# Kernel optimization log

Measured on AMD Instinct MI355X. Metric: run time of the kernel, lower is better.

## Reference

```python
import jax, jax.numpy as jnp
import numpy as np

L = 512       # sequence length
N_AA = 21     # amino-acid alphabet size
D = 128       # per-residue substitution embedding dim
N1 = 256
N2 = 256


def setup_inputs() -> dict:
    key = jax.random.key(0)
    k1, k2, k3 = jax.random.split(key, 3)
    X1 = jax.random.randint(k1, (N1, L), 0, N_AA)
    X2 = jax.random.randint(k2, (N2, L), 0, N_AA)
    W = jax.random.normal(k3, (L * N_AA, N_AA * D), dtype=jnp.float32) * 0.02
    b = jnp.zeros((N_AA * D,), jnp.float32)
    w_param = jnp.zeros((L * (L - 1) // 2,), jnp.float32)
    a = jnp.ones((1,), jnp.float32)
    return {"X1": X1, "X2": X2, "W": W, "b": b, "w_param": w_param, "a": a}


def _network(X, W, b):
    # one-hot + linear stand-in for self.network; outputs (n, n_aa, d)
    n = X.shape[0]
    oh = jax.nn.one_hot(X, N_AA, dtype=W.dtype).reshape(n, -1)  # (n, L*n_aa)
    return (oh @ W + b).reshape(n, N_AA, -1)


def _wdk(subs, w):
    # torch: (subs[:, graph] * w).sum(2) * subs, summed over dim 1
    # graph[i] = arange(L), so this equals subs @ w^T contracted with subs:
    # out[..] = sum_i sum_j subs[.., i] * w[i, j] * subs[.., j]
    return jnp.einsum('...i,ij,...j->...', subs, w, subs)


def reference(X1, X2, W, b, w_param, a):
    n1, Lx = X1.shape
    n2 = X2.shape[0]

    # symmetric pairwise weight matrix; diagonal stays 0 -> sigmoid(0)=0.5
    i_x, i_y = np.tril_indices(Lx, k=-1)
    wm = jnp.zeros((Lx, Lx), W.dtype).at[i_x, i_y].set(w_param).at[i_y, i_x].set(w_param)
    w = jax.nn.sigmoid(wm)

    # per-sequence substitution matrices S = E E^T, (n, n_aa, n_aa)
    E1 = _network(X1, W, b)
    S1 = jnp.einsum('nad,nbd->nab', E1, E1)
    E2 = _network(X2, W, b)
    S2 = jnp.einsum('nad,nbd->nab', E2, E2)

    r1 = jnp.arange(n1)
    r2 = jnp.arange(n2)

    # self terms: subs[n, l] = S[n, X[n,l], X[n,l]]
    d1 = S1[r1[:, None], X1, X1]                  # (n1, L)
    k1 = _wdk(d1, w)[:, None]                     # (n1, 1)
    d2 = S2[r2[:, None], X2, X2]                  # (n2, L)
    k2 = _wdk(d2, w)[None, :]                     # (1, n2)

    # cross terms: average of the two sequences' S, gathered directly
    # (avoids materializing the (n1*n2, n_aa, n_aa) averaged S tensor)
    g1 = S1[r1[:, None, None], X1[:, None, :], X2[None, :, :]]  # (n1, n2, L)
    g2 = S2[r2[None, :, None], X1[:, None, :], X2[None, :, :]]  # (n1, n2, L)
    subs = 0.5 * (g1 + g2)

    K = _wdk(subs, w)                             # (n1, n2)
    K = K / jnp.sqrt(k1) / jnp.sqrt(k2)
    return (a ** 2) * K
```

## Files before the change

kernel.cpp:

```cpp
#include <hip/hip_runtime.h>
#include <cstdint>
#include <cstddef>

typedef __attribute__((ext_vector_type(8))) __bf16 bf16x8;
typedef __attribute__((ext_vector_type(4))) float f32x4;
typedef __attribute__((ext_vector_type(16))) float f32x16;

__device__ __forceinline__ unsigned short f2b(float x) {
    uint32_t u = __float_as_uint(x);
    u += 0x7FFFu + ((u >> 16) & 1u);
    return (unsigned short)(u >> 16);
}
__device__ __forceinline__ float b2f(unsigned short h) {
    return __uint_as_float(((uint32_t)h) << 16);
}

#define L_SEQ 512
#define N_AA 21
#define DDIM 128
#define NCOL 2688
#define NSEQ 512
#define TBSTRIDE 448
#define KTOT 10752
#define KWORDS_TOT 336
#define ZCH 12
#define KCHUNK 896
#define KWORDS 28
#define KBTOT 672
#define NFRAG 56448

#define PB_WBZ   14112
#define PB_EINIT 5376
#define PB_REPACK 1024
#define PB_WBUILD 1024
#define PB_ABITS 672
#define PB_TOTAL (PB_WBZ + PB_EINIT + PB_REPACK + PB_WBUILD + PB_ABITS)

__global__ __launch_bounds__(256) void prep_kernel(const int* X1, const int* X2,
                                                   const float* W, const float* bvec, const float* wp,
                                                   uint8_t* X8, uint32_t* Abits,
                                                   float* w32, unsigned short* wswz,
                                                   float* E, unsigned short* Wbz) {
    int bid = blockIdx.x;
    int t = threadIdx.x;
    if (bid < PB_WBZ) {
        int f = bid * 4 + (t >> 6);
        int lane = t & 63, lr = lane & 31, hf = lane >> 5;
        int cb = f / KBTOT, kb = f - cb * KBTOT;
        const float* src = W + (size_t)(kb * 16 + hf * 8) * NCOL + cb * 32 + lr;
        union { uint4 q; unsigned short s[8]; } o;
#pragma unroll
        for (int j = 0; j < 8; ++j) o.s[j] = f2b(src[(size_t)j * NCOL]);
        *(uint4*)&Wbz[(size_t)f * 512 + lane * 8] = o.q;
        return;
    }
    bid -= PB_WBZ;
    if (bid < PB_EINIT) {
        int e = bid * 256 + t;
        E[e] = bvec[e % NCOL];
        return;
    }
    bid -= PB_EINIT;
    if (bid < PB_REPACK) {
        int e = bid * 256 + t;
        if (e < 131072) X8[e] = (uint8_t)X1[e];
        else            X8[e] = (uint8_t)X2[e - 131072];
        return;
    }
    bid -= PB_REPACK;
    if (bid < PB_WBUILD) {
        int e = bid * 256 + t;
        int p = e >> 9, q = e & 511;
        float x = 0.0f;
        if (p > q)      x = wp[p * (p - 1) / 2 + q];
        else if (p < q) x = wp[q * (q - 1) / 2 + p];
        float s = 1.0f / (1.0f + expf(-x));
        w32[e] = s;
        int nb = p >> 5, lr = p & 31;
        int kb = q >> 4, hf = (q >> 3) & 1, j = q & 7;
        wswz[(size_t)((nb * 32 + kb) * 512) + (hf * 32 + lr) * 8 + j] = f2b(s);
        return;
    }
    bid -= PB_WBUILD;
    {
        int e = bid * 256 + t;
        if (e >= NSEQ * KWORDS_TOT) return;
        int seq = e / KWORDS_TOT, w = e - seq * KWORDS_TOT;
        int k0 = w * 32;
        int l_lo = k0 / N_AA;
        int l_hi = (k0 + 31) / N_AA;
        if (l_hi > L_SEQ - 1) l_hi = L_SEQ - 1;
        uint32_t bits = 0;
        for (int l = l_lo; l <= l_hi; ++l) {
            int aa = (seq < 256) ? X1[(size_t)seq * L_SEQ + l]
                                 : X2[(size_t)(seq - 256) * L_SEQ + l];
            int pos = l * N_AA + aa - k0;
            if (pos >= 0 && pos < 32) bits |= (1u << pos);
        }
        Abits[e] = bits;
    }
}

__global__ __launch_bounds__(256) void e_mfma_bz_kernel(const uint32_t* Abits, const unsigned short* Wbz, float* E) {
    __shared__ uint32_t Ab[256 * 29];
    int t = threadIdx.x;
    int c0 = blockIdx.x * 128;
    int m0 = blockIdx.y * 256;
    int w0 = blockIdx.z * KWORDS;

    for (int idx = t; idx < 256 * KWORDS; idx += 256) {
        int r = idx / KWORDS, w = idx - r * KWORDS;
        Ab[r * 29 + w] = Abits[(size_t)(m0 + r) * KWORDS_TOT + w0 + w];
    }
    __syncthreads();

    int wid = t >> 6, lane = t & 63;
    int lr = lane & 31, hf = lane >> 5;
    int mbase = (wid & 1) * 128;

    f32x16 acc[4][2];
#pragma unroll
    for (int s = 0; s < 4; ++s)
#pragma unroll
        for (int o = 0; o < 2; ++o)
#pragma unroll
            for (int r = 0; r < 16; ++r) acc[s][o][r] = 0.f;

    int kb0 = blockIdx.z * (KCHUNK / 16);
    const unsigned short* Bz0 = Wbz + (size_t)(((c0 >> 5) + (wid >> 1) * 2 + 0) * KBTOT + kb0) * 512 + lane * 8;
    const unsigned short* Bz1 = Wbz + (size_t)(((c0 >> 5) + (wid >> 1) * 2 + 1) * KBTOT + kb0) * 512 + lane * 8;

#pragma unroll 2
    for (int ks = 0; ks < KCHUNK / 16; ++ks) {
        int word = ks >> 1;
        int b0 = (ks & 1) * 16 + hf * 8;
        bf16x8 afrag[4];
#pragma unroll
        for (int s = 0; s < 4; ++s) {
            uint32_t bits = Ab[(mbase + s * 32 + lr) * 29 + word];
            uint32_t bb = (bits >> b0) & 0xFFu;
            union { bf16x8 v; uint32_t u[4]; } af;
#pragma unroll
            for (int p = 0; p < 4; ++p) {
                uint32_t u = 0;
                if ((bb >> (2 * p)) & 1u)     u |= 0x3F80u;
                if ((bb >> (2 * p + 1)) & 1u) u |= 0x3F800000u;
                af.u[p] = u;
            }
            afrag[s] = af.v;
        }
        bf16x8 bv0 = *(const bf16x8*)(Bz0 + ks * 512);
        bf16x8 bv1 = *(const bf16x8*)(Bz1 + ks * 512);
#pragma unroll
        for (int s = 0; s < 4; ++s) {
            acc[s][0] = __builtin_amdgcn_mfma_f32_32x32x16_bf16(afrag[s], bv0, acc[s][0], 0, 0, 0);
            acc[s][1] = __builtin_amdgcn_mfma_f32_32x32x16_bf16(afrag[s], bv1, acc[s][1], 0, 0, 0);
        }
    }

#pragma unroll
    for (int s = 0; s < 4; ++s)
#pragma unroll
        for (int o = 0; o < 2; ++o)
#pragma unroll
            for (int r = 0; r < 16; ++r) {
                int row = (r & 3) + 8 * (r >> 2) + 4 * hf;
                float* dst = E + (size_t)(m0 + mbase + s * 32 + row) * NCOL + c0 + ((wid >> 1) * 2) * 32 + (((r >> 4) == 0) ? 0 : 0);
                (void)dst;
                float* dst2 = E + (size_t)(m0 + mbase + s * 32 + row) * NCOL + c0 + ((wid >> 1) * 2 + o) * 32 + lr;
                atomicAdd(dst2, acc[s][o][r]);
            }
}

__global__ __launch_bounds__(256) void t_kernel(const float* E, unsigned short* Tb, float* Tdiag) {
    __shared__ float4 Es4[21 * 33];
    int t = threadIdx.x, n = blockIdx.x;
    for (int e = t; e < 21 * 32; e += 256) {
        int r = e >> 5, d = e & 31;
        Es4[r * 33 + d] = *(const float4*)(E + (size_t)n * NCOL + r * 128 + d * 4);
    }
    __syncthreads();
    for (int e = t; e < 441; e += 256) {
        int r = e / 21, c = e - r * 21;
        const float4* ar = &Es4[r * 33];
        const float4* br = &Es4[c * 33];
        float s = 0.f;
#pragma unroll 8
        for (int d = 0; d < 32; ++d) {
            float4 a = ar[d], b = br[d];
            s += a.x * b.x + a.y * b.y + a.z * b.z + a.w * b.w;
        }
        Tb[(size_t)n * TBSTRIDE + e] = f2b(0.5f * s);
        if (r == c) Tdiag[n * 24 + r] = s;
    }
}

__global__ __launch_bounds__(256) void k_kernel(const uint8_t* X8, const float* Tdiag, const float* w32, float* kinv) {
    __shared__ __align__(16) float dvec[4][512];
    __shared__ float Td[4][21];
    __shared__ float red[4][256];
    int t = threadIdx.x, n0 = blockIdx.x * 4;
    if (t < 84) Td[t / 21][t % 21] = Tdiag[(size_t)(n0 + t / 21) * 24 + (t % 21)];
    __syncthreads();
    for (int e = t; e < 2048; e += 256) {
        int nn = e >> 9, l = e & 511;
        dvec[nn][l] = Td[nn][X8[(size_t)(n0 + nn) * 512 + l]];
    }
    __syncthreads();
    float p0 = 0.f, p1 = 0.f, p2 = 0.f, p3 = 0.f;
    for (int p = t; p < 512; p += 256) {
        const float4* wr4 = (const float4*)(w32 + (size_t)p * 512);
        float d0 = 0.f, d1 = 0.f, d2 = 0.f, d3 = 0.f;
        for (int q = 0; q < 128; ++q) {
            float4 wv = wr4[q];
            float4 a = ((const float4*)dvec[0])[q];
            float4 b = ((const float4*)dvec[1])[q];
            float4 c = ((const float4*)dvec[2])[q];
            float4 d = ((const float4*)dvec[3])[q];
            d0 += wv.x * a.x + wv.y * a.y + wv.z * a.z + wv.w * a.w;
            d1 += wv.x * b.x + wv.y * b.y + wv.z * b.z + wv.w * b.w;
            d2 += wv.x * c.x + wv.y * c.y + wv.z * c.z + wv.w * c.w;
            d3 += wv.x * d.x + wv.y * d.y + wv.z * d.z + wv.w * d.w;
        }
        p0 += dvec[0][p] * d0;
        p1 += dvec[1][p] * d1;
        p2 += dvec[2][p] * d2;
        p3 += dvec[3][p] * d3;
    }
    red[0][t] = p0; red[1][t] = p1; red[2][t] = p2; red[3][t] = p3;
    __syncthreads();
    for (int s = 128; s > 0; s >>= 1) {
        if (t < s) {
            red[0][t] += red[0][t + s];
            red[1][t] += red[1][t + s];
            red[2][t] += red[2][t + s];
            red[3][t] += red[3][t + s];
        }
        __syncthreads();
    }
    if (t < 4) kinv[n0 + t] = 1.0f / sqrtf(red[t][0]);
}

__global__ __launch_bounds__(512, 6) void k4_kernel(const uint8_t* X8, const unsigned short* Tb,
                                                    const unsigned short* wswz, const float* kinv,
                                                    const float* Ainp, float* out) {
    __shared__ unsigned short Sh[32 * 520];
    __shared__ unsigned short Ts1h[4 * TBSTRIDE];
    __shared__ unsigned short Ts2h[8 * TBSTRIDE];
    __shared__ unsigned short A21[4 * 512];
    __shared__ uint8_t Xs2[8 * 512];
    __shared__ float Kacc[8][32];

    int t = threadIdx.x;
    int i0 = blockIdx.x * 4;
    int j0 = blockIdx.y * 8;

    for (int e = t; e < 4 * 512; e += 512)
        A21[e] = (unsigned short)(21 * X8[(size_t)(i0 + (e >> 9)) * 512 + (e & 511)]);
    {
        const uint32_t* s2 = (const uint32_t*)(X8 + (size_t)(256 + j0) * 512);
        uint32_t* d2 = (uint32_t*)Xs2;
        for (int e = t; e < 1024; e += 512) d2[e] = s2[e];
    }
    {
        uint32_t* d1 = (uint32_t*)Ts1h;
        for (int e = t; e < 4 * 224; e += 512) {
            int r = e / 224, w = e - r * 224;
            d1[e] = ((const uint32_t*)(Tb + (size_t)(i0 + r) * TBSTRIDE))[w];
        }
        uint32_t* d2 = (uint32_t*)Ts2h;
        for (int e = t; e < 8 * 224; e += 512) {
            int r = e / 224, w = e - r * 224;
            d2[e] = ((const uint32_t*)(Tb + (size_t)(256 + j0 + r) * TBSTRIDE))[w];
        }
    }
    __syncthreads();

    for (int e4 = t; e4 < 32 * 128; e4 += 512) {
        int pr = e4 >> 7, p = (e4 & 127) * 4;
        int ti = pr >> 3, tj = pr & 7;
        uint64_t a4 = *(const uint64_t*)&A21[ti * 512 + p];
        uint32_t b4 = *(const uint32_t*)&Xs2[tj * 512 + p];
        const unsigned short* T1 = &Ts1h[ti * TBSTRIDE];
        const unsigned short* T2 = &Ts2h[tj * TBSTRIDE];
        uint64_t outw = 0;
#pragma unroll
        for (int u = 0; u < 4; ++u) {
            int idx = (int)((a4 >> (16 * u)) & 0xFFFFu) + (int)((b4 >> (8 * u)) & 0xFFu);
            float v = b2f(T1[idx]) + b2f(T2[idx]);
            outw |= (uint64_t)f2b(v) << (16 * u);
        }
        *(uint64_t*)&Sh[pr * 520 + p] = outw;
    }
    __syncthreads();

    int wid = t >> 6, lane = t & 63;
    int lr = lane & 31, hf = lane >> 5;
    int n_base = wid * 64;

    const unsigned short* Sa = &Sh[lr * 520 + hf * 8];
    const unsigned short* Bz0 = wswz + (size_t)((wid * 2 + 0) * 32) * 512 + lane * 8;
    const unsigned short* Bz1 = wswz + (size_t)((wid * 2 + 1) * 32) * 512 + lane * 8;

    f32x16 acc0, acc1;
#pragma unroll
    for (int j = 0; j < 16; ++j) { acc0[j] = 0.f; acc1[j] = 0.f; }

#pragma unroll 2
    for (int kt = 0; kt < 32; ++kt) {
        bf16x8 av = *(const bf16x8*)(Sa + kt * 16);
        bf16x8 bv0 = *(const bf16x8*)(Bz0 + kt * 512);
        bf16x8 bv1 = *(const bf16x8*)(Bz1 + kt * 512);
        acc0 = __builtin_amdgcn_mfma_f32_32x32x16_bf16(av, bv0, acc0, 0, 0, 0);
        acc1 = __builtin_amdgcn_mfma_f32_32x32x16_bf16(av, bv1, acc1, 0, 0, 0);
    }

    float prow[16];
#pragma unroll
    for (int r = 0; r < 16; ++r) {
        int row = (r & 3) + 8 * (r >> 2) + 4 * hf;
        float v = acc0[r] * b2f(Sh[row * 520 + (n_base + lr)]);
        v      += acc1[r] * b2f(Sh[row * 520 + (n_base + 32 + lr)]);
        prow[r] = v;
    }
#pragma unroll
    for (int r = 0; r < 16; ++r) {
        float v = prow[r];
        v += __shfl_xor(v, 1);
        v += __shfl_xor(v, 2);
        v += __shfl_xor(v, 4);
        v += __shfl_xor(v, 8);
        v += __shfl_xor(v, 16);
        if (lr == 0) {
            int row = (r & 3) + 8 * (r >> 2) + 4 * hf;
            Kacc[wid][row] = v;
        }
    }
    __syncthreads();

    if (t < 32) {
        float K = Kacc[0][t] + Kacc[1][t] + Kacc[2][t] + Kacc[3][t]
                + Kacc[4][t] + Kacc[5][t] + Kacc[6][t] + Kacc[7][t];
        int ti = t >> 3, tj = t & 7;
        int i = i0 + ti, j = j0 + tj;
        float a0 = Ainp[0];
        out[i * 256 + j] = a0 * a0 * K * kinv[i] * kinv[256 + j];
    }
}

extern "C" void kernel_launch(void* const* d_in, const int* in_sizes, int n_in,
                              void* d_out, int out_size, void* d_ws, size_t ws_size,
                              hipStream_t stream) {
    const int*   X1 = (const int*)d_in[0];
    const int*   X2 = (const int*)d_in[1];
    const float* W  = (const float*)d_in[2];
    const float* b  = (const float*)d_in[3];
    const float* wp = (const float*)d_in[4];
    const float* a  = (const float*)d_in[5];
    float* out = (float*)d_out;

    char* ws = (char*)d_ws;
    float*          E     = (float*)(ws + 0);
    unsigned short* Tb    = (unsigned short*)(ws + 5505024);
    float*          Tdiag = (float*)(ws + 5963776);
    float*          w32   = (float*)(ws + 6012928);
    unsigned short* wswz  = (unsigned short*)(ws + 7061504);
    float*          kinv  = (float*)(ws + 7585792);
    uint8_t*        X8    = (uint8_t*)(ws + 7587840);
    uint32_t*       Abits = (uint32_t*)(ws + 7849984);
    unsigned short* Wbz   = (unsigned short*)(ws + 8538112);

    prep_kernel<<<PB_TOTAL, 256, 0, stream>>>(X1, X2, W, b, wp, X8, Abits, w32, wswz, E, Wbz);
    e_mfma_bz_kernel<<<dim3(21, 2, ZCH), 256, 0, stream>>>(Abits, Wbz, E);
    t_kernel<<<512, 256, 0, stream>>>(E, Tb, Tdiag);
    k_kernel<<<128, 256, 0, stream>>>(X8, Tdiag, w32, kinv);
    k4_kernel<<<dim3(64, 32), 512, 0, stream>>>(X8, Tb, wswz, kinv, a, out);
}
```

Measured before the change: 370.2 us.

## Materialize one-hot A as pre-swizzled bf16 fragments and retile the embedding GMM

The embedding GEMM kernel no longer expands a packed bitmask into bf16 A fragments inside the MFMA loop. The prep kernel now writes the one-hot matrix directly in MFMA fragment order as bf16, about 11 MB. The new GEMM launches 1008 blocks over 64x64 warp tiles with 56 k-steps each, reads A and B fragments straight from global memory, uses an XCD-aware block remap, and sets a higher occupancy bound. This removes the per-step ALU and LDS decode work, but adds extra global traffic for A and more atomic adds because the K split is finer.

```diff
diff --git a/kernel.cpp b/kernel.cpp
--- a/kernel.cpp
+++ b/kernel.cpp
@@ -22,25 +22,22 @@
 #define NSEQ 512
 #define TBSTRIDE 448
 #define KTOT 10752
-#define KWORDS_TOT 336
 #define ZCH 12
-#define KCHUNK 896
-#define KWORDS 28
 #define KBTOT 672
-#define NFRAG 56448
+#define KBCH 56
 
 #define PB_WBZ   14112
 #define PB_EINIT 5376
 #define PB_REPACK 1024
 #define PB_WBUILD 1024
-#define PB_ABITS 672
-#define PB_TOTAL (PB_WBZ + PB_EINIT + PB_REPACK + PB_WBUILD + PB_ABITS)
+#define PB_ABZ   2688
+#define PB_TOTAL (PB_WBZ + PB_EINIT + PB_REPACK + PB_WBUILD + PB_ABZ)
 
 __global__ __launch_bounds__(256) void prep_kernel(const int* X1, const int* X2,
                                                    const float* W, const float* bvec, const float* wp,
-                                                   uint8_t* X8, uint32_t* Abits,
+                                                   uint8_t* X8,
                                                    float* w32, unsigned short* wswz,
-                                                   float* E, unsigned short* Wbz) {
+                                                   float* E, unsigned short* Wbz, unsigned short* Abz) {
     int bid = blockIdx.x;
     int t = threadIdx.x;
     if (bid < PB_WBZ) {
@@ -83,93 +80,69 @@
     }
     bid -= PB_WBUILD;
     {
-        int e = bid * 256 + t;
-        if (e >= NSEQ * KWORDS_TOT) return;
-        int seq = e / KWORDS_TOT, w = e - seq * KWORDS_TOT;
-        int k0 = w * 32;
-        int l_lo = k0 / N_AA;
-        int l_hi = (k0 + 31) / N_AA;
-        if (l_hi > L_SEQ - 1) l_hi = L_SEQ - 1;
-        uint32_t bits = 0;
-        for (int l = l_lo; l <= l_hi; ++l) {
-            int aa = (seq < 256) ? X1[(size_t)seq * L_SEQ + l]
-                                 : X2[(size_t)(seq - 256) * L_SEQ + l];
-            int pos = l * N_AA + aa - k0;
-            if (pos >= 0 && pos < 32) bits |= (1u << pos);
-        }
-        Abits[e] = bits;
-    }
-}
-
-__global__ __launch_bounds__(256) void e_mfma_bz_kernel(const uint32_t* Abits, const unsigned short* Wbz, float* E) {
-    __shared__ uint32_t Ab[256 * 29];
-    int t = threadIdx.x;
-    int c0 = blockIdx.x * 128;
-    int m0 = blockIdx.y * 256;
-    int w0 = blockIdx.z * KWORDS;
-
-    for (int idx = t; idx < 256 * KWORDS; idx += 256) {
-        int r = idx / KWORDS, w = idx - r * KWORDS;
-        Ab[r * 29 + w] = Abits[(size_t)(m0 + r) * KWORDS_TOT + w0 + w];
-    }
-    __syncthreads();
-
-    int wid = t >> 6, lane = t & 63;
+        int f = bid * 4 + (t >> 6);
+        int lane = t & 63, lr = lane & 31, hf = lane >> 5;
+        int mb = f / KBTOT, kb = f - mb * KBTOT;
+        int m = mb * 32 + lr;
+        const int* Xrow = (m < 256) ? (X1 + (size_t)m * L_SEQ) : (X2 + (size_t)(m - 256) * L_SEQ);
+        int k0 = kb * 16 + hf * 8;
+        union { uint4 q; unsigned short s[8]; } o;
+#pragma unroll
+        for (int j = 0; j < 8; ++j) {
+            int k = k0 + j;
+            int l = k / N_AA;
+            int aa = k - l * N_AA;
+            o.s[j] = (Xrow[l] == aa) ? (unsigned short)0x3F80u : (unsigned short)0u;
+        }
+        *(uint4*)&Abz[(size_t)f * 512 + lane * 8] = o.q;
+    }
+}
+
+__global__ __launch_bounds__(256, 4) void e_mfma_v2(const unsigned short* Abz, const unsigned short* Wbz, float* E) {
+    int lin = blockIdx.x;
+    int s = ((lin & 7) * 126) + (lin >> 3);
+    int cx = s % 21;
+    int rem = s / 21;
+    int my = rem & 3;
+    int kz = rem >> 2;
+
+    int t = threadIdx.x, wid = t >> 6, lane = t & 63;
     int lr = lane & 31, hf = lane >> 5;
-    int mbase = (wid & 1) * 128;
-
-    f32x16 acc[4][2];
-#pragma unroll
-    for (int s = 0; s < 4; ++s)
-#pragma unroll
-        for (int o = 0; o < 2; ++o)
-#pragma unroll
-            for (int r = 0; r < 16; ++r) acc[s][o][r] = 0.f;
-
-    int kb0 = blockIdx.z * (KCHUNK / 16);
-    const unsigned short* Bz0 = Wbz + (size_t)(((c0 >> 5) + (wid >> 1) * 2 + 0) * KBTOT + kb0) * 512 + lane * 8;
-    const unsigned short* Bz1 = Wbz + (size_t)(((c0 >> 5) + (wid >> 1) * 2 + 1) * KBTOT + kb0) * 512 + lane * 8;
+
+    int kb0 = kz * KBCH;
+    int mb0 = my * 4 + (wid & 1) * 2;
+    int cb0 = cx * 4 + (wid >> 1) * 2;
+
+    const unsigned short* Ap0 = Abz + ((size_t)(mb0 * KBTOT + kb0)) * 512 + lane * 8;
+    const unsigned short* Ap1 = Ap0 + (size_t)KBTOT * 512;
+    const unsigned short* Bp0 = Wbz + ((size_t)(cb0 * KBTOT + kb0)) * 512 + lane * 8;
+    const unsigned short* Bp1 = Bp0 + (size_t)KBTOT * 512;
+
+    f32x16 acc00, acc01, acc10, acc11;
+#pragma unroll
+    for (int r = 0; r < 16; ++r) { acc00[r] = 0.f; acc01[r] = 0.f; acc10[r] = 0.f; acc11[r] = 0.f; }
 
 #pragma unroll 2
-    for (int ks = 0; ks < KCHUNK / 16; ++ks) {
-        int word = ks >> 1;
-        int b0 = (ks & 1) * 16 + hf * 8;
-        bf16x8 afrag[4];
-#pragma unroll
-        for (int s = 0; s < 4; ++s) {
-            uint32_t bits = Ab[(mbase + s * 32 + lr) * 29 + word];
-            uint32_t bb = (bits >> b0) & 0xFFu;
-            union { bf16x8 v; uint32_t u[4]; } af;
-#pragma unroll
-            for (int p = 0; p < 4; ++p) {
-                uint32_t u = 0;
-                if ((bb >> (2 * p)) & 1u)     u |= 0x3F80u;
-                if ((bb >> (2 * p + 1)) & 1u) u |= 0x3F800000u;
-                af.u[p] = u;
-            }
-            afrag[s] = af.v;
-        }
-        bf16x8 bv0 = *(const bf16x8*)(Bz0 + ks * 512);
-        bf16x8 bv1 = *(const bf16x8*)(Bz1 + ks * 512);
-#pragma unroll
-        for (int s = 0; s < 4; ++s) {
-            acc[s][0] = __builtin_amdgcn_mfma_f32_32x32x16_bf16(afrag[s], bv0, acc[s][0], 0, 0, 0);
-            acc[s][1] = __builtin_amdgcn_mfma_f32_32x32x16_bf16(afrag[s], bv1, acc[s][1], 0, 0, 0);
-        }
-    }
-
-#pragma unroll
-    for (int s = 0; s < 4; ++s)
-#pragma unroll
-        for (int o = 0; o < 2; ++o)
-#pragma unroll
-            for (int r = 0; r < 16; ++r) {
-                int row = (r & 3) + 8 * (r >> 2) + 4 * hf;
-                float* dst = E + (size_t)(m0 + mbase + s * 32 + row) * NCOL + c0 + ((wid >> 1) * 2) * 32 + (((r >> 4) == 0) ? 0 : 0);
-                (void)dst;
-                float* dst2 = E + (size_t)(m0 + mbase + s * 32 + row) * NCOL + c0 + ((wid >> 1) * 2 + o) * 32 + lr;
-                atomicAdd(dst2, acc[s][o][r]);
-            }
+    for (int kb = 0; kb < KBCH; ++kb) {
+        bf16x8 a0 = *(const bf16x8*)(Ap0 + kb * 512);
+        bf16x8 a1 = *(const bf16x8*)(Ap1 + kb * 512);
+        bf16x8 b0 = *(const bf16x8*)(Bp0 + kb * 512);
+        bf16x8 b1 = *(const bf16x8*)(Bp1 + kb * 512);
+        acc00 = __builtin_amdgcn_mfma_f32_32x32x16_bf16(a0, b0, acc00, 0, 0, 0);
+        acc01 = __builtin_amdgcn_mfma_f32_32x32x16_bf16(a0, b1, acc01, 0, 0, 0);
+        acc10 = __builtin_amdgcn_mfma_f32_32x32x16_bf16(a1, b0, acc10, 0, 0, 0);
+        acc11 = __builtin_amdgcn_mfma_f32_32x32x16_bf16(a1, b1, acc11, 0, 0, 0);
+    }
+
+#pragma unroll
+    for (int r = 0; r < 16; ++r) {
+        int row = (r & 3) + 8 * (r >> 2) + 4 * hf;
+        float* base = E + (size_t)(mb0 * 32 + row) * NCOL + cb0 * 32 + lr;
+        atomicAdd(base, acc00[r]);
+        atomicAdd(base + 32, acc01[r]);
+        atomicAdd(base + (size_t)32 * NCOL, acc10[r]);
+        atomicAdd(base + (size_t)32 * NCOL + 32, acc11[r]);
+    }
 }
 
 __global__ __launch_bounds__(256) void t_kernel(const float* E, unsigned short* Tb, float* Tdiag) {
@@ -367,11 +340,11 @@
     unsigned short* wswz  = (unsigned short*)(ws + 7061504);
     float*          kinv  = (float*)(ws + 7585792);
     uint8_t*        X8    = (uint8_t*)(ws + 7587840);
-    uint32_t*       Abits = (uint32_t*)(ws + 7849984);
-    unsigned short* Wbz   = (unsigned short*)(ws + 8538112);
-
-    prep_kernel<<<PB_TOTAL, 256, 0, stream>>>(X1, X2, W, b, wp, X8, Abits, w32, wswz, E, Wbz);
-    e_mfma_bz_kernel<<<dim3(21, 2, ZCH), 256, 0, stream>>>(Abits, Wbz, E);
+    unsigned short* Abz   = (unsigned short*)(ws + 7849984);
+    unsigned short* Wbz   = (unsigned short*)(ws + 18860032);
+
+    prep_kernel<<<PB_TOTAL, 256, 0, stream>>>(X1, X2, W, b, wp, X8, w32, wswz, E, Wbz, Abz);
+    e_mfma_v2<<<1008, 256, 0, stream>>>(Abz, Wbz, E);
     t_kernel<<<512, 256, 0, stream>>>(E, Tb, Tdiag);
     k_kernel<<<128, 256, 0, stream>>>(X8, Tdiag, w32, kinv);
     k4_kernel<<<dim3(64, 32), 512, 0, stream>>>(X8, Tb, wswz, kinv, a, out);
```

Measured after the change: 382.7 us. 3.4% more time.

## Retile E matmul with prefetched B and XCD-aware grid; coalesce k_kernel

Applied to the files above, without the earlier changes.

The one-hot embedding GEMM kernel switches from 252 blocks of 256x128 tiles to 1008 blocks of 128x128 tiles. Block indices are remapped so neighbouring blocks are spread across XCDs, and B fragments are software-prefetched four k-steps ahead to hide load latency. Separately, the self-term kernel now has 512 threads, each handling 8 contiguous columns, so w rows are read coalesced and reduced with wave shuffles. This adds more atomicAdd traffic from the smaller tiles in exchange for more parallelism and latency hiding.

```diff
diff --git a/kernel.cpp b/kernel.cpp
--- a/kernel.cpp
+++ b/kernel.cpp
@@ -23,11 +23,10 @@
 #define TBSTRIDE 448
 #define KTOT 10752
 #define KWORDS_TOT 336
+#define KWORDS 28
 #define ZCH 12
-#define KCHUNK 896
-#define KWORDS 28
 #define KBTOT 672
-#define NFRAG 56448
+#define KBCH 56
 
 #define PB_WBZ   14112
 #define PB_EINIT 5376
@@ -101,75 +100,84 @@
     }
 }
 
-__global__ __launch_bounds__(256) void e_mfma_bz_kernel(const uint32_t* Abits, const unsigned short* Wbz, float* E) {
-    __shared__ uint32_t Ab[256 * 29];
-    int t = threadIdx.x;
-    int c0 = blockIdx.x * 128;
-    int m0 = blockIdx.y * 256;
-    int w0 = blockIdx.z * KWORDS;
-
-    for (int idx = t; idx < 256 * KWORDS; idx += 256) {
+__global__ __launch_bounds__(256, 4) void e_mfma_v4(const uint32_t* Abits, const unsigned short* Wbz, float* E) {
+    __shared__ uint32_t Ab[128 * 29];
+
+    int lin = blockIdx.x;
+    int s_ = ((lin & 7) * 126) + (lin >> 3);
+    int cx = s_ % 21;
+    int rem = s_ / 21;
+    int my = rem & 3;
+    int kz = rem >> 2;
+
+    int t = threadIdx.x, wid = t >> 6, lane = t & 63;
+    int lr = lane & 31, hf = lane >> 5, hf8 = hf * 8;
+    int m0 = my * 128;
+    int w0 = kz * KWORDS;
+    int kb0 = kz * KBCH;
+
+    for (int idx = t; idx < 128 * KWORDS; idx += 256) {
         int r = idx / KWORDS, w = idx - r * KWORDS;
         Ab[r * 29 + w] = Abits[(size_t)(m0 + r) * KWORDS_TOT + w0 + w];
     }
     __syncthreads();
 
-    int wid = t >> 6, lane = t & 63;
-    int lr = lane & 31, hf = lane >> 5;
-    int mbase = (wid & 1) * 128;
-
-    f32x16 acc[4][2];
-#pragma unroll
-    for (int s = 0; s < 4; ++s)
-#pragma unroll
-        for (int o = 0; o < 2; ++o)
-#pragma unroll
-            for (int r = 0; r < 16; ++r) acc[s][o][r] = 0.f;
-
-    int kb0 = blockIdx.z * (KCHUNK / 16);
-    const unsigned short* Bz0 = Wbz + (size_t)(((c0 >> 5) + (wid >> 1) * 2 + 0) * KBTOT + kb0) * 512 + lane * 8;
-    const unsigned short* Bz1 = Wbz + (size_t)(((c0 >> 5) + (wid >> 1) * 2 + 1) * KBTOT + kb0) * 512 + lane * 8;
-
-#pragma unroll 2
-    for (int ks = 0; ks < KCHUNK / 16; ++ks) {
-        int word = ks >> 1;
-        int b0 = (ks & 1) * 16 + hf * 8;
-        bf16x8 afrag[4];
-#pragma unroll
-        for (int s = 0; s < 4; ++s) {
-            uint32_t bits = Ab[(mbase + s * 32 + lr) * 29 + word];
-            uint32_t bb = (bits >> b0) & 0xFFu;
-            union { bf16x8 v; uint32_t u[4]; } af;
-#pragma unroll
-            for (int p = 0; p < 4; ++p) {
-                uint32_t u = 0;
-                if ((bb >> (2 * p)) & 1u)     u |= 0x3F80u;
-                if ((bb >> (2 * p + 1)) & 1u) u |= 0x3F800000u;
-                af.u[p] = u;
-            }
-            afrag[s] = af.v;
-        }
-        bf16x8 bv0 = *(const bf16x8*)(Bz0 + ks * 512);
-        bf16x8 bv1 = *(const bf16x8*)(Bz1 + ks * 512);
-#pragma unroll
-        for (int s = 0; s < 4; ++s) {
-            acc[s][0] = __builtin_amdgcn_mfma_f32_32x32x16_bf16(afrag[s], bv0, acc[s][0], 0, 0, 0);
-            acc[s][1] = __builtin_amdgcn_mfma_f32_32x32x16_bf16(afrag[s], bv1, acc[s][1], 0, 0, 0);
-        }
-    }
-
-#pragma unroll
-    for (int s = 0; s < 4; ++s)
-#pragma unroll
-        for (int o = 0; o < 2; ++o)
-#pragma unroll
-            for (int r = 0; r < 16; ++r) {
-                int row = (r & 3) + 8 * (r >> 2) + 4 * hf;
-                float* dst = E + (size_t)(m0 + mbase + s * 32 + row) * NCOL + c0 + ((wid >> 1) * 2) * 32 + (((r >> 4) == 0) ? 0 : 0);
-                (void)dst;
-                float* dst2 = E + (size_t)(m0 + mbase + s * 32 + row) * NCOL + c0 + ((wid >> 1) * 2 + o) * 32 + lr;
-                atomicAdd(dst2, acc[s][o][r]);
-            }
+    int cb = cx * 4 + wid;
+    const unsigned short* Bp = Wbz + ((size_t)(cb * KBTOT + kb0)) * 512 + lane * 8;
+
+    f32x16 acc0, acc1, acc2, acc3;
+#pragma unroll
+    for (int r = 0; r < 16; ++r) { acc0[r] = 0.f; acc1[r] = 0.f; acc2[r] = 0.f; acc3[r] = 0.f; }
+
+    bf16x8 br0 = *(const bf16x8*)(Bp + 0 * 512);
+    bf16x8 br1 = *(const bf16x8*)(Bp + 1 * 512);
+    bf16x8 br2 = *(const bf16x8*)(Bp + 2 * 512);
+    bf16x8 br3 = *(const bf16x8*)(Bp + 3 * 512);
+
+#define AFRAG(S, WORD, SH) ({ \
+        uint32_t bits_ = Ab[((S) * 32 + lr) * 29 + (WORD)]; \
+        uint32_t bb_ = (bits_ >> (SH)) & 0xFFu; \
+        union { bf16x8 v; uint32_t u[4]; } af_; \
+        af_.u[0] = ((bb_ & 1u)   ? 0x3F80u : 0u) | ((bb_ & 2u)   ? 0x3F800000u : 0u); \
+        af_.u[1] = ((bb_ & 4u)   ? 0x3F80u : 0u) | ((bb_ & 8u)   ? 0x3F800000u : 0u); \
+        af_.u[2] = ((bb_ & 16u)  ? 0x3F80u : 0u) | ((bb_ & 32u)  ? 0x3F800000u : 0u); \
+        af_.u[3] = ((bb_ & 64u)  ? 0x3F80u : 0u) | ((bb_ & 128u) ? 0x3F800000u : 0u); \
+        af_.v; })
+
+#define STEP(BV, KB) do { \
+        int word_ = (KB) >> 1; \
+        int sh_ = ((KB) & 1) * 16 + hf8; \
+        acc0 = __builtin_amdgcn_mfma_f32_32x32x16_bf16(AFRAG(0, word_, sh_), BV, acc0, 0, 0, 0); \
+        acc1 = __builtin_amdgcn_mfma_f32_32x32x16_bf16(AFRAG(1, word_, sh_), BV, acc1, 0, 0, 0); \
+        acc2 = __builtin_amdgcn_mfma_f32_32x32x16_bf16(AFRAG(2, word_, sh_), BV, acc2, 0, 0, 0); \
+        acc3 = __builtin_amdgcn_mfma_f32_32x32x16_bf16(AFRAG(3, word_, sh_), BV, acc3, 0, 0, 0); \
+    } while (0)
+
+#pragma unroll 1
+    for (int kb = 0; kb < 48; kb += 4) {
+        STEP(br0, kb + 0); br0 = *(const bf16x8*)(Bp + (size_t)(kb + 4) * 512);
+        STEP(br1, kb + 1); br1 = *(const bf16x8*)(Bp + (size_t)(kb + 5) * 512);
+        STEP(br2, kb + 2); br2 = *(const bf16x8*)(Bp + (size_t)(kb + 6) * 512);
+        STEP(br3, kb + 3); br3 = *(const bf16x8*)(Bp + (size_t)(kb + 7) * 512);
+    }
+    STEP(br0, 48); br0 = *(const bf16x8*)(Bp + 52 * 512);
+    STEP(br1, 49); br1 = *(const bf16x8*)(Bp + 53 * 512);
+    STEP(br2, 50); br2 = *(const bf16x8*)(Bp + 54 * 512);
+    STEP(br3, 51); br3 = *(const bf16x8*)(Bp + 55 * 512);
+    STEP(br0, 52); STEP(br1, 53); STEP(br2, 54); STEP(br3, 55);
+
+#undef STEP
+#undef AFRAG
+
+#pragma unroll
+    for (int r = 0; r < 16; ++r) {
+        int row = (r & 3) + 8 * (r >> 2) + 4 * hf;
+        float* b0p = E + (size_t)(m0 + row) * NCOL + cb * 32 + lr;
+        atomicAdd(b0p, acc0[r]);
+        atomicAdd(b0p + 32 * NCOL, acc1[r]);
+        atomicAdd(b0p + 64 * NCOL, acc2[r]);
+        atomicAdd(b0p + 96 * NCOL, acc3[r]);
+    }
 }
 
 __global__ __launch_bounds__(256) void t_kernel(const float* E, unsigned short* Tb, float* Tdiag) {
@@ -195,50 +203,64 @@
     }
 }
 
-__global__ __launch_bounds__(256) void k_kernel(const uint8_t* X8, const float* Tdiag, const float* w32, float* kinv) {
+__global__ __launch_bounds__(512) void k_kernel(const uint8_t* X8, const float* Tdiag, const float* w32, float* kinv) {
     __shared__ __align__(16) float dvec[4][512];
     __shared__ float Td[4][21];
-    __shared__ float red[4][256];
+    __shared__ float wred[4][8];
     int t = threadIdx.x, n0 = blockIdx.x * 4;
     if (t < 84) Td[t / 21][t % 21] = Tdiag[(size_t)(n0 + t / 21) * 24 + (t % 21)];
     __syncthreads();
-    for (int e = t; e < 2048; e += 256) {
+    for (int e = t; e < 2048; e += 512) {
         int nn = e >> 9, l = e & 511;
         dvec[nn][l] = Td[nn][X8[(size_t)(n0 + nn) * 512 + l]];
     }
     __syncthreads();
-    float p0 = 0.f, p1 = 0.f, p2 = 0.f, p3 = 0.f;
-    for (int p = t; p < 512; p += 256) {
-        const float4* wr4 = (const float4*)(w32 + (size_t)p * 512);
-        float d0 = 0.f, d1 = 0.f, d2 = 0.f, d3 = 0.f;
-        for (int q = 0; q < 128; ++q) {
-            float4 wv = wr4[q];
-            float4 a = ((const float4*)dvec[0])[q];
-            float4 b = ((const float4*)dvec[1])[q];
-            float4 c = ((const float4*)dvec[2])[q];
-            float4 d = ((const float4*)dvec[3])[q];
-            d0 += wv.x * a.x + wv.y * a.y + wv.z * a.z + wv.w * a.w;
-            d1 += wv.x * b.x + wv.y * b.y + wv.z * b.z + wv.w * b.w;
-            d2 += wv.x * c.x + wv.y * c.y + wv.z * c.z + wv.w * c.w;
-            d3 += wv.x * d.x + wv.y * d.y + wv.z * d.z + wv.w * d.w;
-        }
-        p0 += dvec[0][p] * d0;
-        p1 += dvec[1][p] * d1;
-        p2 += dvec[2][p] * d2;
-        p3 += dvec[3][p] * d3;
-    }
-    red[0][t] = p0; red[1][t] = p1; red[2][t] = p2; red[3][t] = p3;
-    __syncthreads();
-    for (int s = 128; s > 0; s >>= 1) {
-        if (t < s) {
-            red[0][t] += red[0][t + s];
-            red[1][t] += red[1][t + s];
-            red[2][t] += red[2][t + s];
-            red[3][t] += red[3][t + s];
-        }
-        __syncthreads();
-    }
-    if (t < 4) kinv[n0 + t] = 1.0f / sqrtf(red[t][0]);
+    int wid = t >> 6, lane = t & 63;
+    int q0 = lane * 8;
+
+    float4 dA0 = *(const float4*)&dvec[0][q0], dA1 = *(const float4*)&dvec[0][q0 + 4];
+    float4 dB0 = *(const float4*)&dvec[1][q0], dB1 = *(const float4*)&dvec[1][q0 + 4];
+    float4 dC0 = *(const float4*)&dvec[2][q0], dC1 = *(const float4*)&dvec[2][q0 + 4];
+    float4 dD0 = *(const float4*)&dvec[3][q0], dD1 = *(const float4*)&dvec[3][q0 + 4];
+
+    float4 rA0 = {0,0,0,0}, rA1 = {0,0,0,0}, rB0 = {0,0,0,0}, rB1 = {0,0,0,0};
+    float4 rC0 = {0,0,0,0}, rC1 = {0,0,0,0}, rD0 = {0,0,0,0}, rD1 = {0,0,0,0};
+
+#define FMA4(R, W, S) do { (R).x += (W).x * (S); (R).y += (W).y * (S); (R).z += (W).z * (S); (R).w += (W).w * (S); } while (0)
+    for (int p = wid; p < 512; p += 8) {
+        const float4* wr = (const float4*)(w32 + (size_t)p * 512 + q0);
+        float4 w0v = wr[0], w1v = wr[1];
+        float a = dvec[0][p], b = dvec[1][p], c = dvec[2][p], d = dvec[3][p];
+        FMA4(rA0, w0v, a); FMA4(rA1, w1v, a);
+        FMA4(rB0, w0v, b); FMA4(rB1, w1v, b);
+        FMA4(rC0, w0v, c); FMA4(rC1, w1v, c);
+        FMA4(rD0, w0v, d); FMA4(rD1, w1v, d);
+    }
+#undef FMA4
+
+#define DOT8(R0, R1, D0, D1) ((R0).x*(D0).x + (R0).y*(D0).y + (R0).z*(D0).z + (R0).w*(D0).w + \
+                              (R1).x*(D1).x + (R1).y*(D1).y + (R1).z*(D1).z + (R1).w*(D1).w)
+    float s0 = DOT8(rA0, rA1, dA0, dA1);
+    float s1 = DOT8(rB0, rB1, dB0, dB1);
+    float s2 = DOT8(rC0, rC1, dC0, dC1);
+    float s3 = DOT8(rD0, rD1, dD0, dD1);
+#undef DOT8
+
+#pragma unroll
+    for (int off = 1; off < 64; off <<= 1) {
+        s0 += __shfl_xor(s0, off);
+        s1 += __shfl_xor(s1, off);
+        s2 += __shfl_xor(s2, off);
+        s3 += __shfl_xor(s3, off);
+    }
+    if (lane == 0) { wred[0][wid] = s0; wred[1][wid] = s1; wred[2][wid] = s2; wred[3][wid] = s3; }
+    __syncthreads();
+    if (t < 4) {
+        float kk = 0.f;
+#pragma unroll
+        for (int w = 0; w < 8; ++w) kk += wred[t][w];
+        kinv[n0 + t] = 1.0f / sqrtf(kk);
+    }
 }
 
 __global__ __launch_bounds__(512, 6) void k4_kernel(const uint8_t* X8, const unsigned short* Tb,
@@ -371,8 +393,8 @@
     unsigned short* Wbz   = (unsigned short*)(ws + 8538112);
 
     prep_kernel<<<PB_TOTAL, 256, 0, stream>>>(X1, X2, W, b, wp, X8, Abits, w32, wswz, E, Wbz);
-    e_mfma_bz_kernel<<<dim3(21, 2, ZCH), 256, 0, stream>>>(Abits, Wbz, E);
+    e_mfma_v4<<<1008, 256, 0, stream>>>(Abits, Wbz, E);
     t_kernel<<<512, 256, 0, stream>>>(E, Tb, Tdiag);
-    k_kernel<<<128, 256, 0, stream>>>(X8, Tdiag, w32, kinv);
+    k_kernel<<<128, 512, 0, stream>>>(X8, Tdiag, w32, kinv);
     k4_kernel<<<dim3(64, 32), 512, 0, stream>>>(X8, Tb, wswz, kinv, a, out);
 }
```

Result: faster. 355.3 us (-4.0%).
